# Optimization experiments

Measured on AMD Instinct MI355X. Metric: run time of the kernel, lower is better.

Reference implementation:

```python
import jax, jax.numpy as jnp
import numpy as np

NUM_STEPS = 10
TEMP = 2.0
EPS = 1e-20
K = 4   # number of codebooks
N = 8   # codes per codebook
E = 16  # code dim


def _grid_flat():
    x = np.linspace(0.0, 1.5, NUM_STEPS)
    g = np.stack(np.meshgrid(x, x, x), axis=-1)  # [10,10,10,3], 'xy' indexing as in torch source
    return jnp.asarray(g.reshape(-1, 3), dtype=jnp.float32)  # [1000, 3]


def _gumbel(key, shape):
    u = jax.random.uniform(key, shape, dtype=jnp.float32)
    return -jnp.log(-jnp.log(u + EPS) + EPS)


def setup_inputs() -> dict:
    key = jax.random.key(0)
    k1, k2, k3, k4, k5 = jax.random.split(key, 5)
    B, S, D = 32, 2048, 64
    inputs = jax.random.normal(k1, (B, S, D), dtype=jnp.float32)
    linear_w = jax.random.normal(k2, (64, 3), dtype=jnp.float32) * 0.5
    linear_b = jax.random.normal(k3, (64,), dtype=jnp.float32) * 0.1
    emb = jax.random.normal(k4, (K * N, E), dtype=jnp.float32)
    emb_spaces = emb / jnp.linalg.norm(emb, axis=-1, keepdims=True)  # F.normalize(p=2, dim=-1)
    lin_ws = jax.random.normal(k5, (K, E, D), dtype=jnp.float32) * (1.0 / np.sqrt(D))
    return {"inputs": inputs, "linear_w": linear_w, "linear_b": linear_b,
            "emb_spaces": emb_spaces, "lin_ws": lin_ws}


def reference(inputs, linear_w, linear_b, emb_spaces, lin_ws):
    B, S, D = inputs.shape
    grid = _grid_flat()                       # [1000, 3]
    vecs = grid @ linear_w.T + linear_b       # [1000, 64]

    kc, kp = jax.random.split(jax.random.key(42))

    # ---- coordinate codebook path ----
    xc = jnp.einsum('bsd,nd->bsn', inputs, vecs)          # [B,S,1000]
    logc = jax.nn.log_softmax(xc, axis=-1)
    log_u_c = jnp.log(jnp.float32(1.0 / NUM_STEPS ** 3))
    # KLDivLoss(log_uniform, logc, log_target=True, batchmean with input.size(0)=1) == full sum
    kl_c = jnp.sum(jnp.exp(logc) * (logc - log_u_c))
    ic = jax.nn.softmax((logc + _gumbel(kc, logc.shape)) / TEMP, axis=-1)
    quantized_coord = jnp.einsum('bsn,nd->bsd', ic, vecs)  # [B,S,64]

    # ---- per-codebook path (all 4 codebooks vectorized; nums are uniform = 8) ----
    h = jnp.einsum('bsd,ked->bske', inputs, lin_ws)        # [B,S,K,E]
    embK = emb_spaces.reshape(K, N, E)                     # contiguous slices of emb_spaces
    xp = jnp.einsum('bske,kne->bskn', h, embK)             # [B,S,K,N]
    logp = jax.nn.log_softmax(xp, axis=-1)
    log_u = jnp.log(jnp.float32(1.0 / N))
    kl_p = jnp.sum(jnp.exp(logp) * (logp - log_u))         # sum over the K per-codebook KLs
    ip = jax.nn.softmax((logp + _gumbel(kp, logp.shape)) / TEMP, axis=-1)
    quantized = jnp.einsum('bskn,kne->bske', ip, embK).reshape(B, S, K * E)  # [B,S,64]

    loss = (kl_c + kl_p) / 5.0
    return (quantized, quantized_coord, loss)
```

## Files before the change

### kernel.cpp

```cpp
#include <hip/hip_runtime.h>
#include <cstdint>

#define NROWS_HALF 32768
#define QC_OFF 4194304
#define LOSS_OFF 8388608

#define U_CH 0
#define U_CL 2048
#define WS_LOSS_BYTE 8192

#define X_STRIDE 68
#define LOG2E 1.4426950408889634f
#define LN2   0.6931471805599453f

typedef short short8 __attribute__((ext_vector_type(8)));
typedef float float4v __attribute__((ext_vector_type(4)));

#define MFMA16(a, b, c) __builtin_amdgcn_mfma_f32_16x16x32_bf16((a), (b), (c), 0, 0, 0)

__device__ uint32_t g_ticket;

__host__ __device__ __forceinline__ void tf2x32(uint32_t k0, uint32_t k1,
                                                uint32_t x0, uint32_t x1,
                                                uint32_t& o0, uint32_t& o1) {
  const uint32_t k2 = k0 ^ k1 ^ 0x1BD11BDAu;
#define TF_R(r) { x0 += x1; x1 = (x1 << (r)) | (x1 >> (32 - (r))); x1 ^= x0; }
  x0 += k0; x1 += k1;
  TF_R(13) TF_R(15) TF_R(26) TF_R(6)
  x0 += k1; x1 += k2 + 1u;
  TF_R(17) TF_R(29) TF_R(16) TF_R(24)
  x0 += k2; x1 += k0 + 2u;
  TF_R(13) TF_R(15) TF_R(26) TF_R(6)
  x0 += k0; x1 += k1 + 3u;
  TF_R(17) TF_R(29) TF_R(16) TF_R(24)
  x0 += k1; x1 += k2 + 4u;
  TF_R(13) TF_R(15) TF_R(26) TF_R(6)
  x0 += k2; x1 += k0 + 5u;
#undef TF_R
  o0 = x0; o1 = x1;
}

__device__ __forceinline__ float rsq_neglog2(uint32_t bits) {
  const float u = __uint_as_float((bits >> 9) | 0x3f800000u) - 1.0f;
  const float l2 = __builtin_amdgcn_logf(u + 1e-20f);
  return __builtin_amdgcn_rsqf(fmaxf(-l2, 1e-20f));
}

__device__ __forceinline__ uint32_t rn16(float f) {
  uint32_t u = __float_as_uint(f);
  return (u + 0x7FFFu + ((u >> 16) & 1u)) >> 16;
}

__device__ __forceinline__ void split2_rn(float f0, float f1, uint32_t& hi, uint32_t& lo) {
  uint32_t h0 = rn16(f0), h1 = rn16(f1);
  hi = h0 | (h1 << 16);
  float l0 = f0 - __uint_as_float(h0 << 16);
  float l1 = f1 - __uint_as_float(h1 << 16);
  lo = rn16(l0) | (rn16(l1) << 16);
}

__device__ __forceinline__ void split8_rn(const float* p, short8& hi, short8& lo) {
  float4 f0 = *(const float4*)p;
  float4 f1 = *(const float4*)(p + 4);
  union { uint32_t u[4]; short8 s; } H, L;
  split2_rn(f0.x, f0.y, H.u[0], L.u[0]);
  split2_rn(f0.z, f0.w, H.u[1], L.u[1]);
  split2_rn(f1.x, f1.y, H.u[2], L.u[2]);
  split2_rn(f1.z, f1.w, H.u[3], L.u[3]);
  hi = H.s; lo = L.s;
}

__device__ __forceinline__ short8 as_s8(uint4 v) {
  union { uint4 u; short8 s; } c; c.u = v; return c.s;
}

__device__ __forceinline__ float4v tile_mfma(const ushort* __restrict__ Vh,
                                             const ushort* __restrict__ Vl,
                                             int nb, const short8* ah, const short8* al) {
  uint4 bh0 = *(const uint4*)(Vh + nb);
  uint4 bl0 = *(const uint4*)(Vl + nb);
  float4v acc = {0.f, 0.f, 0.f, 0.f};
  acc = MFMA16(ah[0], as_s8(bh0), acc);
  acc = MFMA16(ah[0], as_s8(bl0), acc);
  acc = MFMA16(al[0], as_s8(bh0), acc);
  uint4 bh1 = *(const uint4*)(Vh + nb + 32);
  uint4 bl1 = *(const uint4*)(Vl + nb + 32);
  acc = MFMA16(ah[1], as_s8(bh1), acc);
  acc = MFMA16(ah[1], as_s8(bl1), acc);
  acc = MFMA16(al[1], as_s8(bh1), acc);
  return acc;
}

__global__ void setup_kernel(const float* __restrict__ emb, const float* __restrict__ lws,
                             ushort* __restrict__ wsu) {
  int idx = blockIdx.x * 256 + threadIdx.x;
  if (idx < 2048) {
    int m = idx >> 6, c = idx & 63, k = m >> 3;
    float a = 0.f;
    #pragma unroll
    for (int e = 0; e < 16; ++e) a += emb[m * 16 + e] * lws[(k * 16 + e) * 64 + c];
    a *= LOG2E;
    uint32_t h = rn16(a);
    float fl = a - __uint_as_float(h << 16);
    wsu[U_CH + idx] = (ushort)h;
    wsu[U_CL + idx] = (ushort)rn16(fl);
  } else if (idx == 2048) {
    *(float*)((char*)wsu + WS_LOSS_BYTE) = 0.f;
    g_ticket = 0u;
  }
}

__global__ __launch_bounds__(512, 4) void fused_kernel(
    const float* __restrict__ inp, const float* __restrict__ emb,
    const float* __restrict__ lw, const float* __restrict__ lb,
    const ushort* __restrict__ wsu, float* __restrict__ out,
    float* __restrict__ loss_acc,
    uint32_t kc0, uint32_t kc1, uint32_t kp0, uint32_t kp1) {

  __shared__ float x_s[32 * X_STRIDE];
  __shared__ float xp_s[32 * 32];
  __shared__ float4 sq4_s[16 * 3 * 12];
  __shared__ float u_s[32 * 3];
  __shared__ float swq_s[192];
  __shared__ float tq_s[32 * 4];
  __shared__ float emb_s[512];
  __shared__ float wv_s[64 * 16];
  __shared__ float inv_s[128];
  __shared__ float kl_s;

  const int t = threadIdx.x;
  const int lane = t & 63;
  const int w = t >> 6;
  const int q = lane >> 4;
  const int mn = lane & 15;
  const int g0 = blockIdx.x * 16;

  if (t == 0) kl_s = 0.f;
  emb_s[t] = emb[t];

  const float pw0 = lw[lane * 3 + 0];
  const float pw1 = lw[lane * 3 + 1];
  const float pw2 = lw[lane * 3 + 2];

  #pragma unroll
  for (int it = 0; it < 4; ++it) {
    int rl = it * 8 + w;
    int row = (rl < 16) ? (g0 + rl) : (g0 + rl - 16 + NROWS_HALF);
    float v = inp[row * 64 + lane];
    x_s[rl * X_STRIDE + lane] = v;
    float u0 = v * pw0, u1 = v * pw1, u2 = v * pw2;
    #pragma unroll
    for (int off = 32; off > 0; off >>= 1) {
      u0 += __shfl_xor(u0, off);
      u1 += __shfl_xor(u1, off);
      u2 += __shfl_xor(u2, off);
    }
    if (lane == 0) {
      u_s[rl * 3 + 0] = u0; u_s[rl * 3 + 1] = u1; u_s[rl * 3 + 2] = u2;
    }
  }
  __syncthreads();

  if (t < 96) {
    const int row = t & 31, axis = t >> 5;
    const int pair = row & 15, half = row >> 4;
    const float ua = u_s[row * 3 + axis];
    const float b = 1.5f * fmaxf(ua, 0.f);
    float S = 0.f, W = 0.f;
    float2* slotbase = (float2*)&sq4_s[(pair * 3 + axis) * 12];
    #pragma unroll
    for (int i = 0; i < 10; ++i) {
      float gi = (float)(i * (1.5 / 9.0));
      float lg = (ua * gi - b) * LOG2E;
      float P = __builtin_amdgcn_exp2f(lg);
      S += P; W += lg * P;
      slotbase[i * 2 + half] = make_float2(__builtin_amdgcn_sqrtf(P), (float)i);
    }
    slotbase[10 * 2 + half] = make_float2(0.f, 10.f);
    slotbase[11 * 2 + half] = make_float2(0.f, 11.f);
    swq_s[axis * 64 + row * 2 + 0] = S;
    swq_s[axis * 64 + row * 2 + 1] = W;
  }

  short8 ah[2], al[2];
  const bool codew = (w < 2) || (w >= 6);
  const int rt = (w >= 6) ? 1 : 0;
  const int ct = (w < 2) ? w : (w - 6);
  if (codew) {
    #pragma unroll
    for (int s = 0; s < 2; ++s)
      split8_rn(&x_s[(rt * 16 + mn) * X_STRIDE + s * 32 + q * 8], ah[s], al[s]);
  }
  __syncthreads();

  if (t < 32) {
    float Sa = swq_s[t * 2],       Wa = swq_s[t * 2 + 1];
    float Sb = swq_s[64 + t * 2],  Wb = swq_s[64 + t * 2 + 1];
    float Sc = swq_s[128 + t * 2], Wc = swq_s[128 + t * 2 + 1];
    float kl = LN2 * ((Wa * __builtin_amdgcn_rcpf(Sa) +
                       Wb * __builtin_amdgcn_rcpf(Sb) +
                       Wc * __builtin_amdgcn_rcpf(Sc)) -
                      __builtin_amdgcn_logf(Sa * Sb * Sc)) + 6.9077552789821f;
    atomicAdd(&kl_s, kl);
  }

  if (codew) {
    float4v acc = tile_mfma(wsu + U_CH, wsu + U_CL, (ct * 16 + mn) * 64 + q * 8, ah, al);
    #pragma unroll
    for (int r = 0; r < 4; ++r)
      xp_s[(rt * 16 + q * 4 + r) * 32 + ct * 16 + mn] = acc[r];
  }

  float T[16];
  #pragma unroll
  for (int z = 0; z < 16; ++z) T[z] = 0.f;

  #pragma unroll
  for (int pp = 0; pp < 2; ++pp) {
    const int p = w + pp * 8;
    const uint32_t jb = (uint32_t)(g0 + p) * 1000u;
    const float4* base4 = &sq4_s[p * 36];
    float t0l = 0.f, t1l = 0.f, t2l = 0.f, t3l = 0.f;
    float t0h = 0.f, t1h = 0.f, t2h = 0.f, t3h = 0.f;
    #pragma unroll 2
    for (int it = 0; it < 16; ++it) {
      int c = it * 64 + lane;
      uint32_t y0, y1;
      tf2x32(kc0, kc1, jb + (uint32_t)c, jb + (uint32_t)c + 32768000u, y0, y1);
      int d10 = (c * 6554) >> 16;
      int iy  = (c * 656) >> 16;
      int kz  = c - d10 * 10;
      int jx  = d10 - iy * 10;
      float4 a4 = base4[jx], b4 = base4[12 + iy], c4 = base4[24 + kz];
      float rL = rsq_neglog2(y0);
      float rH = rsq_neglog2(y1);
      float wL = a4.x * b4.x * (c4.x * rL);
      float wH = a4.z * b4.z * (c4.z * rH);
      t0l += wL; t1l += wL * a4.y; t2l += wL * b4.y; t3l += wL * c4.y;
      t0h += wH; t1h += wH * a4.y; t2h += wH * b4.y; t3h += wH * c4.y;
    }
    T[pp * 8 + 0] = t0l; T[pp * 8 + 1] = t1l; T[pp * 8 + 2] = t2l; T[pp * 8 + 3] = t3l;
    T[pp * 8 + 4] = t0h; T[pp * 8 + 5] = t1h; T[pp * 8 + 6] = t2h; T[pp * 8 + 7] = t3h;
  }

  #pragma unroll
  for (int off = 32; off > 0; off >>= 1) {
    #pragma unroll
    for (int z = 0; z < 16; ++z) T[z] += __shfl_xor(T[z], off);
  }
  if (lane == 0) {
    #pragma unroll
    for (int pp = 0; pp < 2; ++pp) {
      int rl = w + pp * 8, rh = rl + 16;
      #pragma unroll
      for (int cmp = 0; cmp < 4; ++cmp) {
        tq_s[rl * 4 + cmp] = T[pp * 8 + cmp];
        tq_s[rh * 4 + cmp] = T[pp * 8 + 4 + cmp];
      }
    }
  }
  __syncthreads();

  {
    const int d = t & 63, rb = t >> 6;
    const float l0 = lw[d * 3 + 0], l1 = lw[d * 3 + 1], l2 = lw[d * 3 + 2];
    const float lbd = lb[d];
    const float stepf = (float)(1.5 / 9.0);
    #pragma unroll
    for (int kk = 0; kk < 4; ++kk) {
      int m = rb + kk * 8;
      float T0v = tq_s[m * 4 + 0], T1v = tq_s[m * 4 + 1];
      float T2v = tq_s[m * 4 + 2], T3v = tq_s[m * 4 + 3];
      float num = (T1v * l0 + T2v * l1 + T3v * l2) * stepf + T0v * lbd;
      int grow = (m < 16) ? (g0 + m) : (g0 + m - 16 + NROWS_HALF);
      out[QC_OFF + grow * 64 + d] = num * __builtin_amdgcn_rcpf(T0v);
    }
  }

  {
    const int u_ = t >> 3, n = t & 7;
    const int p = u_ >> 2, k = u_ & 3;
    const float xpA = xp_s[p * 32 + k * 8 + n];
    const float xpB = xp_s[(p + 16) * 32 + k * 8 + n];
    float mA = xpA, mB = xpB;
    #pragma unroll
    for (int off = 1; off < 8; off <<= 1) {
      mA = fmaxf(mA, __shfl_xor(mA, off));
      mB = fmaxf(mB, __shfl_xor(mB, off));
    }
    float eA = __builtin_amdgcn_exp2f(xpA - mA);
    float eB = __builtin_amdgcn_exp2f(xpB - mB);
    float s0A = eA, s1A = eA * xpA, s0B = eB, s1B = eB * xpB;
    const uint32_t base = (uint32_t)(g0 + p) * 32u + (uint32_t)k * 8u;
    uint32_t y0, y1;
    tf2x32(kp0, kp1, base + (uint32_t)n, base + (uint32_t)n + 1048576u, y0, y1);
    float wvA = __builtin_amdgcn_exp2f((xpA - mA) * 0.5f) * rsq_neglog2(y0);
    float wvB = __builtin_amdgcn_exp2f((xpB - mB) * 0.5f) * rsq_neglog2(y1);
    float swA = wvA, swB = wvB;
    #pragma unroll
    for (int off = 1; off < 8; off <<= 1) {
      s0A += __shfl_xor(s0A, off);
      s1A += __shfl_xor(s1A, off);
      s0B += __shfl_xor(s0B, off);
      s1B += __shfl_xor(s1B, off);
      swA += __shfl_xor(swA, off);
      swB += __shfl_xor(swB, off);
    }
    wv_s[u_ * 16 + n] = wvA;
    wv_s[u_ * 16 + 8 + n] = wvB;
    if (n == 0) {
      inv_s[u_ * 2 + 0] = __builtin_amdgcn_rcpf(swA);
      inv_s[u_ * 2 + 1] = __builtin_amdgcn_rcpf(swB);
      atomicAdd(&kl_s,
          LN2 * ((s1A * __builtin_amdgcn_rcpf(s0A) - mA) - __builtin_amdgcn_logf(s0A)) +
          LN2 * ((s1B * __builtin_amdgcn_rcpf(s0B) - mB) - __builtin_amdgcn_logf(s0B)) +
          4.1588830833596715f);
    }
  }
  __syncthreads();

  float* q_s = x_s;
  {
    const int r = t >> 4, e = t & 15;
    const int p = r & 15, h = r >> 4;
    #pragma unroll
    for (int k = 0; k < 4; ++k) {
      const int u_ = p * 4 + k;
      float aa = 0.f;
      #pragma unroll
      for (int n = 0; n < 8; ++n)
        aa += wv_s[u_ * 16 + h * 8 + n] * emb_s[(k * 8 + n) * 16 + e];
      q_s[r * X_STRIDE + k * 16 + e] = aa * inv_s[u_ * 2 + h];
    }
  }
  __syncthreads();

  #pragma unroll
  for (int it = 0; it < 4; ++it) {
    int idx = it * 512 + t;
    int rl = idx >> 6, c = idx & 63;
    int row = (rl < 16) ? (g0 + rl) : (g0 + rl - 16 + NROWS_HALF);
    out[row * 64 + c] = q_s[rl * X_STRIDE + c];
  }
  if (t == 0) {
    atomicAdd(loss_acc, kl_s);
    __threadfence();
    uint32_t tk = atomicAdd(&g_ticket, 1u);
    if (tk == 2047u) {
      __threadfence();
      out[LOSS_OFF] = atomicAdd(loss_acc, 0.0f) * 0.2f;
    }
  }
}

extern "C" void kernel_launch(void* const* d_in, const int* in_sizes, int n_in,
                              void* d_out, int out_size, void* d_ws, size_t ws_size,
                              hipStream_t stream) {
  const float* inp  = (const float*)d_in[0];
  const float* lw   = (const float*)d_in[1];
  const float* lb   = (const float*)d_in[2];
  const float* emb  = (const float*)d_in[3];
  const float* lws  = (const float*)d_in[4];
  float* out = (float*)d_out;
  ushort* wsu = (ushort*)d_ws;
  float* loss = (float*)((char*)d_ws + WS_LOSS_BYTE);

  uint32_t a0, b0, a1, b1;
  tf2x32(0u, 42u, 0u, 2u, a0, b0);
  tf2x32(0u, 42u, 1u, 3u, a1, b1);
  const uint32_t kc0 = a0, kc1 = a1;
  const uint32_t kp0 = b0, kp1 = b1;

  setup_kernel<<<9, 256, 0, stream>>>(emb, lws, wsu);
  fused_kernel<<<2048, 512, 0, stream>>>(inp, emb, lw, lb, wsu, out, loss,
                                         kc0, kc1, kp0, kp1);
}
```

Before: 219.8 us.

## Fold codebook projection setup into fused kernel and simplify Gumbel uniform math

Removes the separate setup kernel by having every block compute the emb×lin_ws code matrix (hi/lo bf16 split) into shared memory, and replaces the setup's loss/ticket reset with a hipMemsetAsync on the workspace. It also computes the Gumbel uniform with an int-to-float convert and an fma, replacing the bit-cast and subtract, and drops a clamp. The aim is to save the extra kernel launch and its dependency. The cost is redundant per-block compute across 2048 blocks, 8 KB more LDS that may reduce occupancy, and a memset node that may itself cost about as much as a small kernel.

```diff
diff --git a/kernel.cpp b/kernel.cpp
--- a/kernel.cpp
+++ b/kernel.cpp
@@ -5,10 +5,6 @@
 #define QC_OFF 4194304
 #define LOSS_OFF 8388608
 
-#define U_CH 0
-#define U_CL 2048
-#define WS_LOSS_BYTE 8192
-
 #define X_STRIDE 68
 #define LOG2E 1.4426950408889634f
 #define LN2   0.6931471805599453f
@@ -17,8 +13,6 @@
 typedef float float4v __attribute__((ext_vector_type(4)));
 
 #define MFMA16(a, b, c) __builtin_amdgcn_mfma_f32_16x16x32_bf16((a), (b), (c), 0, 0, 0)
-
-__device__ uint32_t g_ticket;
 
 __host__ __device__ __forceinline__ void tf2x32(uint32_t k0, uint32_t k1,
                                                 uint32_t x0, uint32_t x1,
@@ -41,9 +35,10 @@
 }
 
 __device__ __forceinline__ float rsq_neglog2(uint32_t bits) {
-  const float u = __uint_as_float((bits >> 9) | 0x3f800000u) - 1.0f;
-  const float l2 = __builtin_amdgcn_logf(u + 1e-20f);
-  return __builtin_amdgcn_rsqf(fmaxf(-l2, 1e-20f));
+  const float uf = (float)(bits >> 9);
+  const float l2 = __builtin_amdgcn_logf(
+      __builtin_fmaf(uf, 1.1920928955078125e-7f, 1e-20f));
+  return __builtin_amdgcn_rsqf(-l2);
 }
 
 __device__ __forceinline__ uint32_t rn16(float f) {
@@ -74,8 +69,7 @@
   union { uint4 u; short8 s; } c; c.u = v; return c.s;
 }
 
-__device__ __forceinline__ float4v tile_mfma(const ushort* __restrict__ Vh,
-                                             const ushort* __restrict__ Vl,
+__device__ __forceinline__ float4v tile_mfma(const ushort* Vh, const ushort* Vl,
                                              int nb, const short8* ah, const short8* al) {
   uint4 bh0 = *(const uint4*)(Vh + nb);
   uint4 bl0 = *(const uint4*)(Vl + nb);
@@ -91,30 +85,11 @@
   return acc;
 }
 
-__global__ void setup_kernel(const float* __restrict__ emb, const float* __restrict__ lws,
-                             ushort* __restrict__ wsu) {
-  int idx = blockIdx.x * 256 + threadIdx.x;
-  if (idx < 2048) {
-    int m = idx >> 6, c = idx & 63, k = m >> 3;
-    float a = 0.f;
-    #pragma unroll
-    for (int e = 0; e < 16; ++e) a += emb[m * 16 + e] * lws[(k * 16 + e) * 64 + c];
-    a *= LOG2E;
-    uint32_t h = rn16(a);
-    float fl = a - __uint_as_float(h << 16);
-    wsu[U_CH + idx] = (ushort)h;
-    wsu[U_CL + idx] = (ushort)rn16(fl);
-  } else if (idx == 2048) {
-    *(float*)((char*)wsu + WS_LOSS_BYTE) = 0.f;
-    g_ticket = 0u;
-  }
-}
-
 __global__ __launch_bounds__(512, 4) void fused_kernel(
     const float* __restrict__ inp, const float* __restrict__ emb,
     const float* __restrict__ lw, const float* __restrict__ lb,
-    const ushort* __restrict__ wsu, float* __restrict__ out,
-    float* __restrict__ loss_acc,
+    const float* __restrict__ lws, float* __restrict__ out,
+    float* __restrict__ loss_ws,
     uint32_t kc0, uint32_t kc1, uint32_t kp0, uint32_t kp1) {
 
   __shared__ float x_s[32 * X_STRIDE];
@@ -126,6 +101,8 @@
   __shared__ float emb_s[512];
   __shared__ float wv_s[64 * 16];
   __shared__ float inv_s[128];
+  __shared__ alignas(16) ushort code_hi[2048];
+  __shared__ alignas(16) ushort code_lo[2048];
   __shared__ float kl_s;
 
   const int t = threadIdx.x;
@@ -160,6 +137,23 @@
     }
   }
   __syncthreads();
+
+  {
+    const int c = t & 63, mrow = t >> 6;
+    #pragma unroll
+    for (int j = 0; j < 4; ++j) {
+      const int m = mrow + j * 8;
+      float a = 0.f;
+      #pragma unroll
+      for (int e = 0; e < 16; ++e)
+        a += emb_s[m * 16 + e] * lws[(j * 16 + e) * 64 + c];
+      a *= LOG2E;
+      uint32_t h = rn16(a);
+      float fl = a - __uint_as_float(h << 16);
+      code_hi[m * 64 + c] = (ushort)h;
+      code_lo[m * 64 + c] = (ushort)rn16(fl);
+    }
+  }
 
   if (t < 96) {
     const int row = t & 31, axis = t >> 5;
@@ -205,7 +199,7 @@
   }
 
   if (codew) {
-    float4v acc = tile_mfma(wsu + U_CH, wsu + U_CL, (ct * 16 + mn) * 64 + q * 8, ah, al);
+    float4v acc = tile_mfma(code_hi, code_lo, (ct * 16 + mn) * 64 + q * 8, ah, al);
     #pragma unroll
     for (int r = 0; r < 4; ++r)
       xp_s[(rt * 16 + q * 4 + r) * 32 + ct * 16 + mn] = acc[r];
@@ -343,12 +337,12 @@
     out[row * 64 + c] = q_s[rl * X_STRIDE + c];
   }
   if (t == 0) {
-    atomicAdd(loss_acc, kl_s);
+    atomicAdd(loss_ws, kl_s);
     __threadfence();
-    uint32_t tk = atomicAdd(&g_ticket, 1u);
+    uint32_t tk = atomicAdd((uint32_t*)loss_ws + 1, 1u);
     if (tk == 2047u) {
       __threadfence();
-      out[LOSS_OFF] = atomicAdd(loss_acc, 0.0f) * 0.2f;
+      out[LOSS_OFF] = atomicAdd(loss_ws, 0.0f) * 0.2f;
     }
   }
 }
@@ -362,8 +356,7 @@
   const float* emb  = (const float*)d_in[3];
   const float* lws  = (const float*)d_in[4];
   float* out = (float*)d_out;
-  ushort* wsu = (ushort*)d_ws;
-  float* loss = (float*)((char*)d_ws + WS_LOSS_BYTE);
+  float* loss_ws = (float*)d_ws;
 
   uint32_t a0, b0, a1, b1;
   tf2x32(0u, 42u, 0u, 2u, a0, b0);
@@ -371,7 +364,7 @@
   const uint32_t kc0 = a0, kc1 = a1;
   const uint32_t kp0 = b0, kp1 = b1;
 
-  setup_kernel<<<9, 256, 0, stream>>>(emb, lws, wsu);
-  fused_kernel<<<2048, 512, 0, stream>>>(inp, emb, lw, lb, wsu, out, loss,
+  hipMemsetAsync(d_ws, 0, 8, stream);
+  fused_kernel<<<2048, 512, 0, stream>>>(inp, emb, lw, lb, lws, out, loss_ws,
                                          kc0, kc1, kp0, kp1);
 }
```

Measured after the change: 232.5 us. 1.06x slower.
